# Performance work log

Hardware: AMD Instinct MI355X
Metric: run time of the kernel (lower is better)

The kernel has to match this reference:

```python
import jax, jax.numpy as jnp
import numpy as np

HEAD_SIZE = 64
N_EMB = 384
B, S = 512, 256

def setup_inputs() -> dict:
    key = jax.random.key(0)
    k1, k2, k3, k4 = jax.random.split(key, 4)
    x = jax.random.normal(k1, (B, S, N_EMB), dtype=jnp.float32)
    scale = 1.0 / np.sqrt(N_EMB)
    Wq = jax.random.normal(k2, (N_EMB, HEAD_SIZE), dtype=jnp.float32) * scale
    Wk = jax.random.normal(k3, (N_EMB, HEAD_SIZE), dtype=jnp.float32) * scale
    Wv = jax.random.normal(k4, (N_EMB, HEAD_SIZE), dtype=jnp.float32) * scale
    return {"x": x, "Wq": Wq, "Wk": Wk, "Wv": Wv}

def reference(x, Wq, Wk, Wv):
    # Projections (Linear, no bias): [B,S,E] @ [E,H] -> [B,S,H]
    q = jnp.einsum('bse,eh->bsh', x, Wq)
    k = jnp.einsum('bse,eh->bsh', x, Wk)
    v = jnp.einsum('bse,eh->bsh', x, Wv)
    # Scores: [B,S,S], scaled by 1/sqrt(head_size)
    scores = jnp.einsum('bqh,bkh->bqk', q, k) / jnp.sqrt(jnp.asarray(HEAD_SIZE, x.dtype))
    seq_len = x.shape[1]
    causal = jnp.tril(jnp.ones((seq_len, seq_len), dtype=bool))
    scores = jnp.where(causal[None, :, :], scores, jnp.asarray(-jnp.inf, scores.dtype))
    attn = jax.nn.softmax(scores, axis=-1)
    # dropout_ratio=0 -> identity
    out = jnp.einsum('bqk,bkh->bqh', attn, v)
    return out
```

## Files before the change

kernel.cpp:

```cpp
#include <hip/hip_runtime.h>
#include <hip/hip_bf16.h>


#define NB   512
#define SS   256
#define EE   384
#define HH   64

#define PR16  16
#define LROW  392
#define XLSZ  (PR16 * LROW)

#define SYNC_LDS() asm volatile("s_waitcnt lgkmcnt(0)\n\ts_barrier" ::: "memory")

typedef short bf16x8 __attribute__((ext_vector_type(8)));
typedef float f32x4  __attribute__((ext_vector_type(4)));

__device__ __forceinline__ short f2bf(float f) {
  union { float f; unsigned u; } x; x.f = f;
  unsigned r = x.u + 0x7fffu + ((x.u >> 16) & 1u);
  return (short)(r >> 16);
}

__global__ __launch_bounds__(256) void prep_w_kernel(
    const float* __restrict__ Wq, const float* __restrict__ Wk,
    const float* __restrict__ Wv, short* __restrict__ wfrag) {
  int t = blockIdx.x * 256 + threadIdx.x;
  if (t >= 12 * 12 * 64) return;
  int ks  = t / (12 * 64);
  int rem = t % (12 * 64);
  int nf  = rem / 64;
  int l   = rem % 64;
  int l15 = l & 15, lhi = l >> 4;
  int ncat = nf * 16 + l15;
  const float* W = (ncat < 64) ? Wq : (ncat < 128 ? Wk : Wv);
  int n = ncat & 63;
  short* dst = wfrag + (size_t)t * 8;
#pragma unroll
  for (int j = 0; j < 8; ++j) {
    int kk = ks * 32 + lhi * 8 + j;
    dst[j] = f2bf(W[kk * 64 + n]);
  }
}

__global__ __launch_bounds__(768, 3) void fused_kernel(
    const float* __restrict__ x, const short* __restrict__ wfrag,
    float* __restrict__ out) {
  __shared__ __align__(16) short Ql[SS * HH];
  __shared__ __align__(16) short Kl[SS * HH];
  __shared__ __align__(16) short Vt[HH * SS];
  __shared__ __align__(16) short xst[2 * XLSZ];

  int b    = blockIdx.x;
  int tid  = threadIdx.x;
  int lane = tid & 63, wv = tid >> 6;
  int l15  = lane & 15, lhi = lane >> 4;
  int sw   = l15 & 7;
  const float* xb = x + (size_t)b * SS * EE;

  bf16x8 af[12];
#pragma unroll
  for (int ks = 0; ks < 12; ++ks)
    af[ks] = *(const bf16x8*)(wfrag + ((size_t)(ks * 12 + wv) * 64 + lane) * 8);
#pragma unroll
  for (int ks = 0; ks < 12; ++ks)
    asm volatile("" : "+v"(af[ks]));

  f32x4 st[2];
  auto loadch = [&](int ch) {
    const float* p0 = xb + (size_t)ch * PR16 * EE;
    const f32x4* p = (const f32x4*)(p0 + (size_t)tid * 8);
    st[0] = p[0];
    st[1] = p[1];
  };
  auto writech = [&](short* xl) {
    int row = tid / 48, cg = tid % 48;
    union { bf16x8 vv; __hip_bfloat162 h2[4]; } u;
    u.h2[0] = __float22bfloat162_rn(make_float2(st[0][0], st[0][1]));
    u.h2[1] = __float22bfloat162_rn(make_float2(st[0][2], st[0][3]));
    u.h2[2] = __float22bfloat162_rn(make_float2(st[1][0], st[1][1]));
    u.h2[3] = __float22bfloat162_rn(make_float2(st[1][2], st[1][3]));
    *(bf16x8*)(xl + row * LROW + cg * 8) = u.vv;
  };

  loadch(0);
  writech(xst);
  for (int ch = 0; ch < 16; ++ch) {
    if (ch < 15) loadch(ch + 1);
    SYNC_LDS();
    const short* xl = xst + (ch & 1) * XLSZ;

    f32x4 acc = (f32x4){0.f, 0.f, 0.f, 0.f};
#pragma unroll
    for (int ks = 0; ks < 12; ++ks) {
      bf16x8 bx = *(const bf16x8*)(xl + l15 * LROW + ks * 32 + lhi * 8);
      acc = __builtin_amdgcn_mfma_f32_16x16x32_bf16(af[ks], bx, acc, 0, 0, 0);
    }

    int row  = ch * PR16 + l15;
    int srow = ((row & 8) >> 1) | (row & 3);
    int ncat = wv * 16 + lhi * 4;
    if (wv < 4) {
      union { short4 s4; __hip_bfloat162 h2[2]; } oq;
      oq.h2[0] = __float22bfloat162_rn(make_float2(acc[0], acc[1]));
      oq.h2[1] = __float22bfloat162_rn(make_float2(acc[2], acc[3]));
      *(short4*)(Ql + row * 64 + (ncat ^ ((row & 7) << 3))) = oq.s4;
    } else if (wv < 8) {
      int col = ncat - 64;
      union { short4 s4; __hip_bfloat162 h2[2]; } ok;
      ok.h2[0] = __float22bfloat162_rn(make_float2(acc[0], acc[1]));
      ok.h2[1] = __float22bfloat162_rn(make_float2(acc[2], acc[3]));
      *(short4*)(Kl + row * 64 + (col ^ (srow << 3))) = ok.s4;
    } else {
#pragma unroll
      for (int j = 0; j < 4; ++j) {
        int h = ncat - 128 + j;
        Vt[h * 256 + (row ^ ((h & 7) << 3))] = f2bf(acc[j]);
      }
    }
    if (ch < 15) writech(xst + ((ch + 1) & 1) * XLSZ);
  }
  SYNC_LDS();

  int nt, rt0 = 0, rt1 = 0;
  if (wv < 4)       { nt = 1; rt0 = 15 - wv; }
  else if (wv < 10) { nt = 2; rt0 = 15 - wv; rt1 = wv - 4; }
  else              { nt = 0; }

  size_t obase = (size_t)b * SS * HH;
  for (int u = 0; u < nt; ++u) {
    int rt    = (u == 0) ? rt0 : rt1;
    int qrow0 = rt * 16;
    int twp   = (rt + 2) & ~1;
    int nk    = twp >> 1;
    int qg    = qrow0 + l15;

    int qlrow = qrow0 + l15;
    bf16x8 qa0 = *(const bf16x8*)(Ql + qlrow * 64 + ((lhi * 8) ^ ((qlrow & 7) << 3)));
    bf16x8 qa1 = *(const bf16x8*)(Ql + qlrow * 64 + ((32 + lhi * 8) ^ ((qlrow & 7) << 3)));

    f32x4 s[16];
#pragma unroll
    for (int t = 0; t < 16; ++t) {
      if (t >= twp) continue;
      int kc = (t >> 1) * 32 + ((l15 >> 2) << 3) + ((t & 1) << 2) + (l15 & 3);
      const short* kp = Kl + kc * 64;
      bf16x8 kb0 = *(const bf16x8*)(kp + ((lhi * 8) ^ (sw << 3)));
      bf16x8 kb1 = *(const bf16x8*)(kp + ((32 + lhi * 8) ^ (sw << 3)));
      __builtin_amdgcn_s_setprio(1);
      f32x4 a = (f32x4){0.f, 0.f, 0.f, 0.f};
      a = __builtin_amdgcn_mfma_f32_16x16x32_bf16(kb0, qa0, a, 0, 0, 0);
      a = __builtin_amdgcn_mfma_f32_16x16x32_bf16(kb1, qa1, a, 0, 0, 0);
      __builtin_amdgcn_s_setprio(0);
#pragma unroll
      for (int r = 0; r < 4; ++r) {
        int kg = (t >> 1) * 32 + lhi * 8 + ((t & 1) << 2) + r;
        s[t][r] = (kg <= qg) ? a[r] * 0.125f : -INFINITY;
      }
    }

    float mx = -3.0e38f;
#pragma unroll
    for (int t = 0; t < 16; ++t) {
      if (t >= twp) continue;
#pragma unroll
      for (int r = 0; r < 4; ++r) mx = fmaxf(mx, s[t][r]);
    }
    mx = fmaxf(mx, __shfl_xor(mx, 16));
    mx = fmaxf(mx, __shfl_xor(mx, 32));
    float sm = 0.f;
#pragma unroll
    for (int t = 0; t < 16; ++t) {
      if (t >= twp) continue;
#pragma unroll
      for (int r = 0; r < 4; ++r) {
        float p = __expf(s[t][r] - mx);
        s[t][r] = p;
        sm += p;
      }
    }
    sm += __shfl_xor(sm, 16);
    sm += __shfl_xor(sm, 32);
    float inv = 1.f / sm;
    float invq[4];
#pragma unroll
    for (int r = 0; r < 4; ++r) invq[r] = __shfl(inv, lhi * 4 + r);

    f32x4 o[4];
#pragma unroll
    for (int nf = 0; nf < 4; ++nf) o[nf] = (f32x4){0.f, 0.f, 0.f, 0.f};
#pragma unroll
    for (int kc2 = 0; kc2 < 8; ++kc2) {
      if (kc2 >= nk) continue;
      union { bf16x8 v; __hip_bfloat162 h2[4]; } pu;
      pu.h2[0] = __float22bfloat162_rn(make_float2(s[2*kc2][0],   s[2*kc2][1]));
      pu.h2[1] = __float22bfloat162_rn(make_float2(s[2*kc2][2],   s[2*kc2][3]));
      pu.h2[2] = __float22bfloat162_rn(make_float2(s[2*kc2+1][0], s[2*kc2+1][1]));
      pu.h2[3] = __float22bfloat162_rn(make_float2(s[2*kc2+1][2], s[2*kc2+1][3]));
      int kofs = kc2 * 32 + lhi * 8;
      __builtin_amdgcn_s_setprio(1);
#pragma unroll
      for (int nf = 0; nf < 4; ++nf) {
        int hrow = nf * 16 + l15;
        bf16x8 vb = *(const bf16x8*)(Vt + hrow * 256 + (kofs ^ ((hrow & 7) << 3)));
        o[nf] = __builtin_amdgcn_mfma_f32_16x16x32_bf16(pu.v, vb, o[nf], 0, 0, 0);
      }
      __builtin_amdgcn_s_setprio(0);
    }

#pragma unroll
    for (int nf = 0; nf < 4; ++nf)
#pragma unroll
      for (int r = 0; r < 4; ++r) {
        int q = qrow0 + lhi * 4 + r;
        int h = nf * 16 + l15;
        out[obase + (size_t)q * HH + h] = o[nf][r] * invq[r];
      }
  }
}

extern "C" void kernel_launch(void* const* d_in, const int* in_sizes, int n_in,
                              void* d_out, int out_size, void* d_ws, size_t ws_size,
                              hipStream_t stream) {
  const float* x  = (const float*)d_in[0];
  const float* Wq = (const float*)d_in[1];
  const float* Wk = (const float*)d_in[2];
  const float* Wv = (const float*)d_in[3];
  float* out = (float*)d_out;

  short* wfrag = (short*)d_ws;

  prep_w_kernel<<<36, 256, 0, stream>>>(Wq, Wk, Wv, wfrag);
  fused_kernel<<<512, 768, 0, stream>>>(x, wfrag, out);
}
```

Before: 56.61 us.

## Interleave per-tile causal attention into projection loop with two-pass recomputed softmax

Instead of running all attention after the Q/K/V projection, each chunk iteration has one wave compute attention for the previous 16-row query tile, trying to overlap attention with projecting the next chunk. The softmax is restructured into a max pass and a second pass that recomputes QK^T, applies exp, and feeds the PV MFMAs directly, so the 16-entry score register array is gone. This cuts register pressure but doubles the QK^T MFMAs. It also assigns each tile to one wave per chunk, so waves may stall at barriers behind it. Masked key and value rows of the current chunk may be read while still being written.

```diff
diff --git a/kernel.cpp b/kernel.cpp
--- a/kernel.cpp
+++ b/kernel.cpp
@@ -57,6 +57,7 @@
   int l15  = lane & 15, lhi = lane >> 4;
   int sw   = l15 & 7;
   const float* xb = x + (size_t)b * SS * EE;
+  size_t obase = (size_t)b * SS * HH;
 
   bf16x8 af[12];
 #pragma unroll
@@ -83,6 +84,97 @@
     *(bf16x8*)(xl + row * LROW + cg * 8) = u.vv;
   };
 
+  auto attn_tile = [&](int rt) {
+    int qrow0 = rt * 16;
+    int twp   = (rt + 2) & ~1;
+    int nk    = twp >> 1;
+    int qg    = qrow0 + l15;
+
+    int qlrow = qrow0 + l15;
+    bf16x8 qa0 = *(const bf16x8*)(Ql + qlrow * 64 + ((lhi * 8) ^ ((qlrow & 7) << 3)));
+    bf16x8 qa1 = *(const bf16x8*)(Ql + qlrow * 64 + ((32 + lhi * 8) ^ ((qlrow & 7) << 3)));
+
+    float mx = -3.0e38f;
+    for (int t = 0; t < twp; ++t) {
+      int kc = (t >> 1) * 32 + ((l15 >> 2) << 3) + ((t & 1) << 2) + (l15 & 3);
+      const short* kp = Kl + kc * 64;
+      bf16x8 kb0 = *(const bf16x8*)(kp + ((lhi * 8) ^ (sw << 3)));
+      bf16x8 kb1 = *(const bf16x8*)(kp + ((32 + lhi * 8) ^ (sw << 3)));
+      __builtin_amdgcn_s_setprio(1);
+      f32x4 a = (f32x4){0.f, 0.f, 0.f, 0.f};
+      a = __builtin_amdgcn_mfma_f32_16x16x32_bf16(kb0, qa0, a, 0, 0, 0);
+      a = __builtin_amdgcn_mfma_f32_16x16x32_bf16(kb1, qa1, a, 0, 0, 0);
+      __builtin_amdgcn_s_setprio(0);
+#pragma unroll
+      for (int r = 0; r < 4; ++r) {
+        int kg = (t >> 1) * 32 + lhi * 8 + ((t & 1) << 2) + r;
+        float v = a[r] * 0.125f;
+        mx = (kg <= qg) ? fmaxf(mx, v) : mx;
+      }
+    }
+    mx = fmaxf(mx, __shfl_xor(mx, 16));
+    mx = fmaxf(mx, __shfl_xor(mx, 32));
+
+    float sm = 0.f;
+    f32x4 o[4];
+#pragma unroll
+    for (int nf = 0; nf < 4; ++nf) o[nf] = (f32x4){0.f, 0.f, 0.f, 0.f};
+    for (int kc2 = 0; kc2 < nk; ++kc2) {
+      int kcA = kc2 * 32 + ((l15 >> 2) << 3) + (l15 & 3);
+      const short* kpA = Kl + kcA * 64;
+      const short* kpB = kpA + 4 * 64;
+      bf16x8 a0 = *(const bf16x8*)(kpA + ((lhi * 8) ^ (sw << 3)));
+      bf16x8 a1 = *(const bf16x8*)(kpA + ((32 + lhi * 8) ^ (sw << 3)));
+      bf16x8 b0 = *(const bf16x8*)(kpB + ((lhi * 8) ^ (sw << 3)));
+      bf16x8 b1 = *(const bf16x8*)(kpB + ((32 + lhi * 8) ^ (sw << 3)));
+      __builtin_amdgcn_s_setprio(1);
+      f32x4 aA = (f32x4){0.f, 0.f, 0.f, 0.f};
+      aA = __builtin_amdgcn_mfma_f32_16x16x32_bf16(a0, qa0, aA, 0, 0, 0);
+      aA = __builtin_amdgcn_mfma_f32_16x16x32_bf16(a1, qa1, aA, 0, 0, 0);
+      f32x4 aB = (f32x4){0.f, 0.f, 0.f, 0.f};
+      aB = __builtin_amdgcn_mfma_f32_16x16x32_bf16(b0, qa0, aB, 0, 0, 0);
+      aB = __builtin_amdgcn_mfma_f32_16x16x32_bf16(b1, qa1, aB, 0, 0, 0);
+      __builtin_amdgcn_s_setprio(0);
+      float pA[4], pB[4];
+#pragma unroll
+      for (int r = 0; r < 4; ++r) {
+        int kgA = kc2 * 32 + lhi * 8 + r;
+        pA[r] = (kgA <= qg) ? __expf(aA[r] * 0.125f - mx) : 0.f;
+        pB[r] = (kgA + 4 <= qg) ? __expf(aB[r] * 0.125f - mx) : 0.f;
+        sm += pA[r] + pB[r];
+      }
+      union { bf16x8 v; __hip_bfloat162 h2[4]; } pu;
+      pu.h2[0] = __float22bfloat162_rn(make_float2(pA[0], pA[1]));
+      pu.h2[1] = __float22bfloat162_rn(make_float2(pA[2], pA[3]));
+      pu.h2[2] = __float22bfloat162_rn(make_float2(pB[0], pB[1]));
+      pu.h2[3] = __float22bfloat162_rn(make_float2(pB[2], pB[3]));
+      int kofs = kc2 * 32 + lhi * 8;
+      __builtin_amdgcn_s_setprio(1);
+#pragma unroll
+      for (int nf = 0; nf < 4; ++nf) {
+        int hrow = nf * 16 + l15;
+        bf16x8 vb = *(const bf16x8*)(Vt + hrow * 256 + (kofs ^ ((hrow & 7) << 3)));
+        o[nf] = __builtin_amdgcn_mfma_f32_16x16x32_bf16(pu.v, vb, o[nf], 0, 0, 0);
+      }
+      __builtin_amdgcn_s_setprio(0);
+    }
+    sm += __shfl_xor(sm, 16);
+    sm += __shfl_xor(sm, 32);
+    float inv = 1.f / sm;
+    float invq[4];
+#pragma unroll
+    for (int r = 0; r < 4; ++r) invq[r] = __shfl(inv, lhi * 4 + r);
+
+#pragma unroll
+    for (int nf = 0; nf < 4; ++nf)
+#pragma unroll
+      for (int r = 0; r < 4; ++r) {
+        int q = qrow0 + lhi * 4 + r;
+        int h = nf * 16 + l15;
+        out[obase + (size_t)q * HH + h] = o[nf][r] * invq[r];
+      }
+  };
+
   loadch(0);
   writech(xst);
   for (int ch = 0; ch < 16; ++ch) {
@@ -118,105 +210,15 @@
         Vt[h * 256 + (row ^ ((h & 7) << 3))] = f2bf(acc[j]);
       }
     }
+
+    int at = ch - 1;
+    if (at >= 0 && wv == (at % 12)) attn_tile(at);
+
     if (ch < 15) writech(xst + ((ch + 1) & 1) * XLSZ);
   }
   SYNC_LDS();
 
-  int nt, rt0 = 0, rt1 = 0;
-  if (wv < 4)       { nt = 1; rt0 = 15 - wv; }
-  else if (wv < 10) { nt = 2; rt0 = 15 - wv; rt1 = wv - 4; }
-  else              { nt = 0; }
-
-  size_t obase = (size_t)b * SS * HH;
-  for (int u = 0; u < nt; ++u) {
-    int rt    = (u == 0) ? rt0 : rt1;
-    int qrow0 = rt * 16;
-    int twp   = (rt + 2) & ~1;
-    int nk    = twp >> 1;
-    int qg    = qrow0 + l15;
-
-    int qlrow = qrow0 + l15;
-    bf16x8 qa0 = *(const bf16x8*)(Ql + qlrow * 64 + ((lhi * 8) ^ ((qlrow & 7) << 3)));
-    bf16x8 qa1 = *(const bf16x8*)(Ql + qlrow * 64 + ((32 + lhi * 8) ^ ((qlrow & 7) << 3)));
-
-    f32x4 s[16];
-#pragma unroll
-    for (int t = 0; t < 16; ++t) {
-      if (t >= twp) continue;
-      int kc = (t >> 1) * 32 + ((l15 >> 2) << 3) + ((t & 1) << 2) + (l15 & 3);
-      const short* kp = Kl + kc * 64;
-      bf16x8 kb0 = *(const bf16x8*)(kp + ((lhi * 8) ^ (sw << 3)));
-      bf16x8 kb1 = *(const bf16x8*)(kp + ((32 + lhi * 8) ^ (sw << 3)));
-      __builtin_amdgcn_s_setprio(1);
-      f32x4 a = (f32x4){0.f, 0.f, 0.f, 0.f};
-      a = __builtin_amdgcn_mfma_f32_16x16x32_bf16(kb0, qa0, a, 0, 0, 0);
-      a = __builtin_amdgcn_mfma_f32_16x16x32_bf16(kb1, qa1, a, 0, 0, 0);
-      __builtin_amdgcn_s_setprio(0);
-#pragma unroll
-      for (int r = 0; r < 4; ++r) {
-        int kg = (t >> 1) * 32 + lhi * 8 + ((t & 1) << 2) + r;
-        s[t][r] = (kg <= qg) ? a[r] * 0.125f : -INFINITY;
-      }
-    }
-
-    float mx = -3.0e38f;
-#pragma unroll
-    for (int t = 0; t < 16; ++t) {
-      if (t >= twp) continue;
-#pragma unroll
-      for (int r = 0; r < 4; ++r) mx = fmaxf(mx, s[t][r]);
-    }
-    mx = fmaxf(mx, __shfl_xor(mx, 16));
-    mx = fmaxf(mx, __shfl_xor(mx, 32));
-    float sm = 0.f;
-#pragma unroll
-    for (int t = 0; t < 16; ++t) {
-      if (t >= twp) continue;
-#pragma unroll
-      for (int r = 0; r < 4; ++r) {
-        float p = __expf(s[t][r] - mx);
-        s[t][r] = p;
-        sm += p;
-      }
-    }
-    sm += __shfl_xor(sm, 16);
-    sm += __shfl_xor(sm, 32);
-    float inv = 1.f / sm;
-    float invq[4];
-#pragma unroll
-    for (int r = 0; r < 4; ++r) invq[r] = __shfl(inv, lhi * 4 + r);
-
-    f32x4 o[4];
-#pragma unroll
-    for (int nf = 0; nf < 4; ++nf) o[nf] = (f32x4){0.f, 0.f, 0.f, 0.f};
-#pragma unroll
-    for (int kc2 = 0; kc2 < 8; ++kc2) {
-      if (kc2 >= nk) continue;
-      union { bf16x8 v; __hip_bfloat162 h2[4]; } pu;
-      pu.h2[0] = __float22bfloat162_rn(make_float2(s[2*kc2][0],   s[2*kc2][1]));
-      pu.h2[1] = __float22bfloat162_rn(make_float2(s[2*kc2][2],   s[2*kc2][3]));
-      pu.h2[2] = __float22bfloat162_rn(make_float2(s[2*kc2+1][0], s[2*kc2+1][1]));
-      pu.h2[3] = __float22bfloat162_rn(make_float2(s[2*kc2+1][2], s[2*kc2+1][3]));
-      int kofs = kc2 * 32 + lhi * 8;
-      __builtin_amdgcn_s_setprio(1);
-#pragma unroll
-      for (int nf = 0; nf < 4; ++nf) {
-        int hrow = nf * 16 + l15;
-        bf16x8 vb = *(const bf16x8*)(Vt + hrow * 256 + (kofs ^ ((hrow & 7) << 3)));
-        o[nf] = __builtin_amdgcn_mfma_f32_16x16x32_bf16(pu.v, vb, o[nf], 0, 0, 0);
-      }
-      __builtin_amdgcn_s_setprio(0);
-    }
-
-#pragma unroll
-    for (int nf = 0; nf < 4; ++nf)
-#pragma unroll
-      for (int r = 0; r < 4; ++r) {
-        int q = qrow0 + lhi * 4 + r;
-        int h = nf * 16 + l15;
-        out[obase + (size_t)q * HH + h] = o[nf][r] * invq[r];
-      }
-  }
+  if (wv == 3) attn_tile(15);
 }
 
 extern "C" void kernel_launch(void* const* d_in, const int* in_sizes, int n_in,
```

Result: slower. 115.9 us (+104.8%).
